# Optimization experiments

Hardware: AMD Instinct MI355X
Metric: run time of the kernel (lower is better)

## Reference

```python
import jax, jax.numpy as jnp
import numpy as np

EMBED_SIZE = 1024
HEADS = 16
HEAD_DIM = EMBED_SIZE // HEADS


def setup_inputs() -> dict:
    key = jax.random.key(0)
    k1, k2, k3, k4 = jax.random.split(key, 4)
    N, L = 4, 2048
    return {
        "values": jax.random.normal(k1, (N, L, EMBED_SIZE), dtype=jnp.float32),
        "keys": jax.random.normal(k2, (N, L, EMBED_SIZE), dtype=jnp.float32),
        "query": jax.random.normal(k3, (N, L, EMBED_SIZE), dtype=jnp.float32),
        "w_out": jax.random.normal(k4, (EMBED_SIZE, EMBED_SIZE), dtype=jnp.float32) * (1.0 / np.sqrt(EMBED_SIZE)),
        "b_out": jnp.zeros((EMBED_SIZE,), dtype=jnp.float32),
    }


def reference(values, keys, query, w_out, b_out):
    N, q_len, _ = query.shape
    v_len = values.shape[1]
    k_len = keys.shape[1]
    # split heads: (N, L, H, D). NOTE: source never applies the per-head
    # q/k/v Linear layers in forward, so raw inputs are used directly.
    v = values.reshape(N, v_len, HEADS, HEAD_DIM)
    k = keys.reshape(N, k_len, HEADS, HEAD_DIM)
    q = query.reshape(N, q_len, HEADS, HEAD_DIM)
    # energy: (N, H, Q, K); scale by sqrt(embed_size) as in the source
    energy = jnp.einsum('nqhd,nkhd->nhqk', q, k)
    attn = jax.nn.softmax(energy / jnp.sqrt(jnp.float32(EMBED_SIZE)), axis=3)
    out = jnp.einsum('nhql,nlhd->nqhd', attn, v).reshape(N, q_len, EMBED_SIZE)
    # fc_out: x @ W.T + b (torch Linear convention)
    return out @ w_out.T + b_out
```

## Files before the change

### kernel.cpp

```cpp
#include <hip/hip_runtime.h>
#include <hip/hip_bf16.h>

#define NB 4
#define LSEQ 2048
#define NH 16
#define HD 64
#define EMB 1024

typedef __attribute__((ext_vector_type(8))) short bf16x8;
typedef __attribute__((ext_vector_type(4))) float f32x4;
typedef __attribute__((ext_vector_type(16))) float f32x16;
typedef __attribute__((ext_vector_type(2))) unsigned int uint2v;

__device__ __forceinline__ unsigned short f2bf(float x) {
    union { float f; unsigned u; } v; v.f = x;
    unsigned r = v.u + 0x7fff + ((v.u >> 16) & 1);
    return (unsigned short)(r >> 16);
}

__device__ __forceinline__ float exp2_fast(float x) {
#if __has_builtin(__builtin_amdgcn_exp2f)
    return __builtin_amdgcn_exp2f(x);
#else
    float r; asm("v_exp_f32 %0, %1\n\ts_nop 1" : "=v"(r) : "v"(x)); return r;
#endif
}

__device__ __forceinline__ unsigned pack_bf2(float lo, float hi) {
    union { __hip_bfloat162 h2; unsigned u; } cv;
    cv.h2 = __float22bfloat162_rn(make_float2(lo, hi));
    return cv.u;
}

__device__ __forceinline__ void plswap(unsigned &a, unsigned &b) {
#if __has_builtin(__builtin_amdgcn_permlane32_swap)
    uint2v r = __builtin_amdgcn_permlane32_swap(a, b, false, false);
    a = r[0]; b = r[1];
#else
    asm volatile("s_nop 0\n\tv_permlane32_swap_b32 %0, %1\n\ts_nop 0"
                 : "+v"(a), "+v"(b));
#endif
}

__device__ __forceinline__ void async16(void* lds, const void* g) {
    __builtin_amdgcn_global_load_lds(
        (const __attribute__((address_space(1))) unsigned int*)g,
        (__attribute__((address_space(3))) unsigned int*)lds, 16, 0, 0);
}

__global__ void wconv_kernel(const float* __restrict__ Wf, unsigned short* __restrict__ Wb) {
    int i = (blockIdx.x * 256 + threadIdx.x) * 4;
    float4 v = *(const float4*)(Wf + i);
    ushort4 o = { f2bf(v.x), f2bf(v.y), f2bf(v.z), f2bf(v.w) };
    *(ushort4*)(Wb + i) = o;
}

__global__ void k_prep(const float* __restrict__ Kf, unsigned short* __restrict__ Kb) {
    int idx = blockIdx.x * 256 + threadIdx.x;
    int c   = idx & 7;
    int key = (idx >> 3) & 2047;
    int h   = (idx >> 14) & 15;
    int n   = idx >> 18;
    const float* src = Kf + (size_t)(n * LSEQ + key) * EMB + h * HD + c * 8;
    float4 a = *(const float4*)src;
    float4 b = *(const float4*)(src + 4);
    unsigned short* dst = Kb + (((size_t)(n * NH + h) * LSEQ + key) << 6)
                             + ((c ^ (key & 7)) << 3);
    ushort4 o0 = { f2bf(a.x), f2bf(a.y), f2bf(a.z), f2bf(a.w) };
    ushort4 o1 = { f2bf(b.x), f2bf(b.y), f2bf(b.z), f2bf(b.w) };
    *(ushort4*)dst = o0;
    *(ushort4*)(dst + 4) = o1;
}

__global__ void v_prep2(const float* __restrict__ Vf, unsigned short* __restrict__ Vt) {
    __shared__ float T[64][65];
    const int tid = threadIdx.x;
    const int b = blockIdx.x;
    const int kt = b & 31, h = (b >> 5) & 15, n = b >> 9;
    const float* src = Vf + (size_t)(n * LSEQ + kt * 64) * EMB + h * HD;
    unsigned short* dst = Vt + ((size_t)b << 12);

    for (int i = tid; i < 1024; i += 256) {
        const int key = i >> 4;
        const int c4  = (i & 15) * 4;
        const float4 v = *(const float4*)(src + (size_t)key * EMB + c4);
        T[key][c4 + 0] = v.x; T[key][c4 + 1] = v.y;
        T[key][c4 + 2] = v.z; T[key][c4 + 3] = v.w;
    }
    __syncthreads();
    for (int i = tid; i < 512; i += 256) {
        const int d = i >> 3, c = i & 7;
        ushort4 o0 = { f2bf(T[c * 8 + 0][d]), f2bf(T[c * 8 + 1][d]),
                       f2bf(T[c * 8 + 2][d]), f2bf(T[c * 8 + 3][d]) };
        ushort4 o1 = { f2bf(T[c * 8 + 4][d]), f2bf(T[c * 8 + 5][d]),
                       f2bf(T[c * 8 + 6][d]), f2bf(T[c * 8 + 7][d]) };
        unsigned short* p = dst + (d << 6) + ((c ^ (d & 7)) << 3);
        *(ushort4*)p = o0;
        *(ushort4*)(p + 4) = o1;
    }
}

__global__ __launch_bounds__(256, 2)
void attn11_kernel(const float* __restrict__ Qq, const unsigned short* __restrict__ Kb,
                   const unsigned short* __restrict__ Vt, unsigned short* __restrict__ X)
{
    __shared__ unsigned short Kl[2][4096];
    __shared__ unsigned short Vl[2][4096];

    const int tid  = threadIdx.x;
    const int lane = tid & 63;
    const int w    = tid >> 6;
    const int l31  = lane & 31;
    const int hl   = lane >> 5;
    const int swz7 = lane & 7;
    const int l    = ((blockIdx.x & 7) << 6) + (blockIdx.x >> 3);
    const int nh   = l >> 3;
    const int qtile = l & 7;
    const int n = nh >> 4, h = nh & 15;
    const int qrow0 = qtile * 256 + w * 64;

    bf16x8 ones;
    #pragma unroll
    for (int e = 0; e < 8; ++e) ones[e] = (short)0x3F80;

    const float qscale = 0.03125f * 1.44269504f;
    bf16x8 qf[2][4];
    #pragma unroll
    for (int g = 0; g < 2; ++g) {
        const float* qp = Qq + (size_t)(n * LSEQ + qrow0 + g * 32 + l31) * EMB + h * HD + hl * 8;
        #pragma unroll
        for (int dk = 0; dk < 4; ++dk) {
            bf16x8 t;
            #pragma unroll
            for (int e = 0; e < 8; ++e) t[e] = (short)f2bf(qp[dk * 16 + e] * qscale);
            qf[g][dk] = t;
        }
    }

    f32x16 oaccT[2][2];
    f32x16 lacc[2];
    #pragma unroll
    for (int g = 0; g < 2; ++g) {
        #pragma unroll
        for (int e = 0; e < 16; ++e) lacc[g][e] = 0.f;
        #pragma unroll
        for (int db = 0; db < 2; ++db)
            #pragma unroll
            for (int e = 0; e < 16; ++e) oaccT[g][db][e] = 0.f;
    }

    const unsigned short* kg0 = Kb + ((size_t)nh << 17);
    const unsigned short* vg0 = Vt + ((size_t)nh << 17);
    const int t8 = tid << 3;

    async16(&Kl[0][t8],        kg0 + t8);
    async16(&Kl[0][t8 + 2048], kg0 + t8 + 2048);
    async16(&Vl[0][t8],        vg0 + t8);
    async16(&Vl[0][t8 + 2048], vg0 + t8 + 2048);
    asm volatile("s_waitcnt vmcnt(0)" ::: "memory");
    __syncthreads();

    int cur = 0;
    for (int kt = 0; kt < LSEQ / 64; ++kt) {
        if (kt + 1 < LSEQ / 64) {
            const unsigned short* kg = kg0 + ((kt + 1) << 12) + t8;
            const unsigned short* vg = vg0 + ((kt + 1) << 12) + t8;
            async16(&Kl[cur ^ 1][t8],        kg);
            async16(&Kl[cur ^ 1][t8 + 2048], kg + 2048);
            async16(&Vl[cur ^ 1][t8],        vg);
            async16(&Vl[cur ^ 1][t8 + 2048], vg + 2048);
        }

        #pragma unroll
        for (int kb = 0; kb < 2; ++kb) {
            f32x16 sk[2];
            #pragma unroll
            for (int g = 0; g < 2; ++g)
                #pragma unroll
                for (int e = 0; e < 16; ++e) sk[g][e] = 0.f;
            #pragma unroll
            for (int dk = 0; dk < 4; ++dk) {
                bf16x8 ka = *(const bf16x8*)&Kl[cur][((kb * 32 + l31) << 6) + (((2 * dk + hl) ^ swz7) << 3)];
                #pragma unroll
                for (int g = 0; g < 2; ++g)
                    sk[g] = __builtin_amdgcn_mfma_f32_32x32x16_bf16(ka, qf[g][dk], sk[g], 0, 0, 0);
            }

            unsigned wgt[2][4][2];
            #pragma unroll
            for (int g = 0; g < 2; ++g) {
                float p[16];
                #pragma unroll
                for (int e = 0; e < 16; ++e) p[e] = exp2_fast(sk[g][e]);
                #pragma unroll
                for (int gg = 0; gg < 4; ++gg) {
                    wgt[g][gg][0] = pack_bf2(p[4 * gg + 0], p[4 * gg + 1]);
                    wgt[g][gg][1] = pack_bf2(p[4 * gg + 2], p[4 * gg + 3]);
                }
                plswap(wgt[g][0][0], wgt[g][1][0]); plswap(wgt[g][0][1], wgt[g][1][1]);
                plswap(wgt[g][2][0], wgt[g][3][0]); plswap(wgt[g][2][1], wgt[g][3][1]);
            }

            #pragma unroll
            for (int ks = 0; ks < 2; ++ks) {
                union { unsigned u[4]; bf16x8 v; } pu[2];
                #pragma unroll
                for (int g = 0; g < 2; ++g) {
                    pu[g].u[0] = wgt[g][2 * ks + 0][0];
                    pu[g].u[1] = wgt[g][2 * ks + 0][1];
                    pu[g].u[2] = wgt[g][2 * ks + 1][0];
                    pu[g].u[3] = wgt[g][2 * ks + 1][1];
                    lacc[g] = __builtin_amdgcn_mfma_f32_32x32x16_bf16(ones, pu[g].v, lacc[g], 0, 0, 0);
                }
                #pragma unroll
                for (int db = 0; db < 2; ++db) {
                    bf16x8 va = *(const bf16x8*)&Vl[cur][((db * 32 + l31) << 6) + (((4 * kb + 2 * ks + hl) ^ swz7) << 3)];
                    #pragma unroll
                    for (int g = 0; g < 2; ++g)
                        oaccT[g][db] = __builtin_amdgcn_mfma_f32_32x32x16_bf16(va, pu[g].v, oaccT[g][db], 0, 0, 0);
                }
            }
        }

        asm volatile("s_waitcnt vmcnt(0)" ::: "memory");
        __syncthreads();
        cur ^= 1;
    }

    #pragma unroll
    for (int g = 0; g < 2; ++g) {
        const float rcp = 1.0f / lacc[g][0];
        unsigned ow0[4][2], ow1[4][2];
        #pragma unroll
        for (int gg = 0; gg < 4; ++gg) {
            ow0[gg][0] = pack_bf2(oaccT[g][0][4 * gg + 0] * rcp, oaccT[g][0][4 * gg + 1] * rcp);
            ow0[gg][1] = pack_bf2(oaccT[g][0][4 * gg + 2] * rcp, oaccT[g][0][4 * gg + 3] * rcp);
            ow1[gg][0] = pack_bf2(oaccT[g][1][4 * gg + 0] * rcp, oaccT[g][1][4 * gg + 1] * rcp);
            ow1[gg][1] = pack_bf2(oaccT[g][1][4 * gg + 2] * rcp, oaccT[g][1][4 * gg + 3] * rcp);
        }
        #pragma unroll
        for (int gg = 0; gg < 4; ++gg) {
            plswap(ow0[gg][0], ow1[gg][0]);
            plswap(ow0[gg][1], ow1[gg][1]);
        }
        unsigned short* xrow = X + (size_t)(n * LSEQ + qrow0 + g * 32 + l31) * EMB + h * HD + hl * 32;
        #pragma unroll
        for (int gg = 0; gg < 4; ++gg) {
            uint4 st = { ow0[gg][0], ow0[gg][1], ow1[gg][0], ow1[gg][1] };
            *(uint4*)(xrow + 8 * gg) = st;
        }
    }
}

#define KPAD 72
#define PPAD 72

__global__ __launch_bounds__(256, 2)
void attn_kernel(const float* __restrict__ Vv, const float* __restrict__ Kk,
                 const float* __restrict__ Qq, unsigned short* __restrict__ X)
{
    __shared__ unsigned short Klds[64 * KPAD];
    __shared__ unsigned short Vtlds[64 * KPAD];
    __shared__ unsigned short Plds[4 * 16 * PPAD];

    const int tid  = threadIdx.x;
    const int lane = tid & 63;
    const int w    = tid >> 6;
    const int l15  = lane & 15;
    const int l4   = lane >> 4;
    const int qtile = blockIdx.x;
    const int nh    = blockIdx.y;
    const int n = nh >> 4, h = nh & 15;

    bf16x8 qf[2];
    {
        const int qrow = qtile * 64 + w * 16 + l15;
        const float* qp = Qq + (size_t)(n * LSEQ + qrow) * EMB + h * HD + l4 * 8;
        for (int kk = 0; kk < 2; ++kk) {
            bf16x8 t;
            #pragma unroll
            for (int e = 0; e < 8; ++e) t[e] = (short)f2bf(qp[kk * 32 + e] * 0.03125f);
            qf[kk] = t;
        }
    }

    f32x4 oacc[4];
    #pragma unroll
    for (int f = 0; f < 4; ++f) oacc[f] = (f32x4){0.f, 0.f, 0.f, 0.f};
    float mrun[4], lrun[4];
    #pragma unroll
    for (int r = 0; r < 4; ++r) { mrun[r] = -1e30f; lrun[r] = 0.f; }

    for (int kt = 0; kt < LSEQ / 64; ++kt) {
        __syncthreads();
        for (int i = tid; i < 1024; i += 256) {
            const int row = i >> 4;
            const int c4  = (i & 15) * 4;
            const size_t gb = (size_t)(n * LSEQ + kt * 64 + row) * EMB + h * HD + c4;
            const float4 kv = *(const float4*)(Kk + gb);
            const float4 vv = *(const float4*)(Vv + gb);
            ushort4 k4 = { f2bf(kv.x), f2bf(kv.y), f2bf(kv.z), f2bf(kv.w) };
            *(ushort4*)&Klds[row * KPAD + c4] = k4;
            Vtlds[(c4 + 0) * KPAD + row] = f2bf(vv.x);
            Vtlds[(c4 + 1) * KPAD + row] = f2bf(vv.y);
            Vtlds[(c4 + 2) * KPAD + row] = f2bf(vv.z);
            Vtlds[(c4 + 3) * KPAD + row] = f2bf(vv.w);
        }
        __syncthreads();

        f32x4 s[4];
        #pragma unroll
        for (int f = 0; f < 4; ++f) {
            f32x4 acc = (f32x4){0.f, 0.f, 0.f, 0.f};
            #pragma unroll
            for (int kk = 0; kk < 2; ++kk) {
                bf16x8 kb = *(const bf16x8*)&Klds[(f * 16 + l15) * KPAD + kk * 32 + l4 * 8];
                acc = __builtin_amdgcn_mfma_f32_16x16x32_bf16(qf[kk], kb, acc, 0, 0, 0);
            }
            s[f] = acc;
        }

        float mnew[4], corr[4];
        #pragma unroll
        for (int r = 0; r < 4; ++r) {
            float m0 = fmaxf(fmaxf(s[0][r], s[1][r]), fmaxf(s[2][r], s[3][r]));
            #pragma unroll
            for (int msk = 1; msk < 16; msk <<= 1) m0 = fmaxf(m0, __shfl_xor(m0, msk));
            mnew[r] = fmaxf(mrun[r], m0);
            corr[r] = __expf(mrun[r] - mnew[r]);
        }
        float psum[4] = {0.f, 0.f, 0.f, 0.f};
        #pragma unroll
        for (int f = 0; f < 4; ++f) {
            #pragma unroll
            for (int r = 0; r < 4; ++r) {
                float p = __expf(s[f][r] - mnew[r]);
                psum[r] += p;
                Plds[(w * 16 + l4 * 4 + r) * PPAD + f * 16 + l15] = f2bf(p);
            }
        }
        #pragma unroll
        for (int r = 0; r < 4; ++r) {
            float t = psum[r];
            #pragma unroll
            for (int msk = 1; msk < 16; msk <<= 1) t += __shfl_xor(t, msk);
            lrun[r] = lrun[r] * corr[r] + t;
            mrun[r] = mnew[r];
        }
        #pragma unroll
        for (int f = 0; f < 4; ++f) {
            #pragma unroll
            for (int r = 0; r < 4; ++r) oacc[f][r] *= corr[r];
        }
        __syncthreads();

        #pragma unroll
        for (int ks = 0; ks < 2; ++ks) {
            bf16x8 pa = *(const bf16x8*)&Plds[(w * 16 + l15) * PPAD + ks * 32 + l4 * 8];
            #pragma unroll
            for (int f = 0; f < 4; ++f) {
                bf16x8 vb = *(const bf16x8*)&Vtlds[(f * 16 + l15) * KPAD + ks * 32 + l4 * 8];
                oacc[f] = __builtin_amdgcn_mfma_f32_16x16x32_bf16(pa, vb, oacc[f], 0, 0, 0);
            }
        }
    }

    #pragma unroll
    for (int f = 0; f < 4; ++f) {
        #pragma unroll
        for (int r = 0; r < 4; ++r) {
            const int qrow = qtile * 64 + w * 16 + l4 * 4 + r;
            const float o = oacc[f][r] / lrun[r];
            X[(size_t)(n * LSEQ + qrow) * EMB + h * HD + f * 16 + l15] = f2bf(o);
        }
    }
}

__global__ __launch_bounds__(256, 2)
void proj4_kernel(const unsigned short* __restrict__ X, const unsigned short* __restrict__ Wb,
                  const float* __restrict__ bias, float* __restrict__ out)
{
    __shared__ unsigned short Al[2][8192];
    __shared__ unsigned short Bl[2][8192];

    const int tid  = threadIdx.x;
    const int lane = tid & 63;
    const int w    = tid >> 6;
    const int l15  = lane & 15;
    const int l4   = lane >> 4;
    const int bid  = blockIdx.x;
    const int bm   = (bid & 7) * 8 + ((bid >> 3) & 7);
    const int bn   = bid >> 6;
    const int wr = (w >> 1) * 64;
    const int wc = (w & 1) * 64;

    f32x4 acc[4][4];
    #pragma unroll
    for (int i = 0; i < 4; ++i)
        #pragma unroll
        for (int j = 0; j < 4; ++j) acc[i][j] = (f32x4){0.f, 0.f, 0.f, 0.f};

    int srow[4], soff[4];
    #pragma unroll
    for (int j = 0; j < 4; ++j) {
        const int cid = tid + j * 256;
        srow[j] = cid >> 3;
        const int c = cid & 7;
        soff[j] = ((c ^ (srow[j] & 7)) << 3);
    }

#define PROJ_STAGE(buf, k0)                                                          \
    {                                                                                \
        _Pragma("unroll")                                                            \
        for (int j = 0; j < 4; ++j) {                                                \
            const int cid = tid + j * 256;                                           \
            async16(&Al[buf][cid << 3],                                              \
                    &X [(size_t)(bm * 128 + srow[j]) * EMB + (k0) + soff[j]]);       \
            async16(&Bl[buf][cid << 3],                                              \
                    &Wb[(size_t)(bn * 128 + srow[j]) * EMB + (k0) + soff[j]]);       \
        }                                                                            \
    }

    PROJ_STAGE(0, 0)
    asm volatile("s_waitcnt vmcnt(0)" ::: "memory");
    __syncthreads();

    int cur = 0;
    for (int k0 = 0; k0 < EMB; k0 += 64) {
        if (k0 + 64 < EMB) PROJ_STAGE(cur ^ 1, k0 + 64)

        #pragma unroll
        for (int kk = 0; kk < 2; ++kk) {
            bf16x8 af[4], bfr[4];
            #pragma unroll
            for (int i = 0; i < 4; ++i) {
                const int row = wr + i * 16 + l15;
                af[i] = *(const bf16x8*)&Al[cur][(row << 6) + (((kk * 4 + l4) ^ (row & 7)) << 3)];
            }
            #pragma unroll
            for (int j = 0; j < 4; ++j) {
                const int row = wc + j * 16 + l15;
                bfr[j] = *(const bf16x8*)&Bl[cur][(row << 6) + (((kk * 4 + l4) ^ (row & 7)) << 3)];
            }
            #pragma unroll
            for (int i = 0; i < 4; ++i)
                #pragma unroll
                for (int j = 0; j < 4; ++j)
                    acc[i][j] = __builtin_amdgcn_mfma_f32_16x16x32_bf16(af[i], bfr[j], acc[i][j], 0, 0, 0);
        }

        asm volatile("s_waitcnt vmcnt(0)" ::: "memory");
        __syncthreads();
        cur ^= 1;
    }

    #pragma unroll
    for (int i = 0; i < 4; ++i) {
        const int row = bm * 128 + wr + i * 16 + l4 * 4;
        #pragma unroll
        for (int j = 0; j < 4; ++j) {
            const int col = bn * 128 + wc + j * 16 + l15;
            const float bj = bias[col];
            #pragma unroll
            for (int r = 0; r < 4; ++r)
                out[(size_t)(row + r) * EMB + col] = acc[i][j][r] + bj;
        }
    }
}

extern "C" void kernel_launch(void* const* d_in, const int* in_sizes, int n_in,
                              void* d_out, int out_size, void* d_ws, size_t ws_size,
                              hipStream_t stream) {
    const float* Vv   = (const float*)d_in[0];
    const float* Kk   = (const float*)d_in[1];
    const float* Qq   = (const float*)d_in[2];
    const float* Wf   = (const float*)d_in[3];
    const float* bias = (const float*)d_in[4];
    float* out = (float*)d_out;

    unsigned short* X  = (unsigned short*)d_ws;
    unsigned short* Wb = (unsigned short*)((char*)d_ws + (size_t)16 * 1024 * 1024);
    const size_t need = (size_t)50 * 1024 * 1024;

    wconv_kernel<<<dim3(EMB * EMB / 1024), 256, 0, stream>>>(Wf, Wb);

    if (ws_size >= need) {
        unsigned short* Kb = (unsigned short*)((char*)d_ws + (size_t)18 * 1024 * 1024);
        unsigned short* Vt = (unsigned short*)((char*)d_ws + (size_t)34 * 1024 * 1024);
        k_prep<<<dim3(4096), 256, 0, stream>>>(Kk, Kb);
        v_prep2<<<dim3(2048), 256, 0, stream>>>(Vv, Vt);
        attn11_kernel<<<dim3(512), 256, 0, stream>>>(Qq, Kb, Vt, X);
    } else {
        attn_kernel<<<dim3(LSEQ / 64, NB * NH), 256, 0, stream>>>(Vv, Kk, Qq, X);
    }

    proj4_kernel<<<dim3(512), 256, 0, stream>>>(X, Wb, bias, out);
}
```

Measured before the change: 131.5 us.

## Merge prep kernels into one launch and halve attention query tile per block

The weight, K and V conversion kernels become a single launch, with blocks dispatched to each job by block index. This removes two kernel launches and the gaps between them. The attention kernel now gives each wave 32 query rows instead of 64, doubling the grid to 1024 blocks and raising the launch bounds occupancy hint to 4. The goal is more parallelism and lower register pressure, at the cost of reusing each staged K/V tile across half as many queries, which doubles K/V traffic through LDS and global memory.

```diff
diff --git a/kernel.cpp b/kernel.cpp
--- a/kernel.cpp
+++ b/kernel.cpp
@@ -55,53 +55,67 @@
     *(ushort4*)(Wb + i) = o;
 }
 
-__global__ void k_prep(const float* __restrict__ Kf, unsigned short* __restrict__ Kb) {
-    int idx = blockIdx.x * 256 + threadIdx.x;
-    int c   = idx & 7;
-    int key = (idx >> 3) & 2047;
-    int h   = (idx >> 14) & 15;
-    int n   = idx >> 18;
-    const float* src = Kf + (size_t)(n * LSEQ + key) * EMB + h * HD + c * 8;
-    float4 a = *(const float4*)src;
-    float4 b = *(const float4*)(src + 4);
-    unsigned short* dst = Kb + (((size_t)(n * NH + h) * LSEQ + key) << 6)
-                             + ((c ^ (key & 7)) << 3);
-    ushort4 o0 = { f2bf(a.x), f2bf(a.y), f2bf(a.z), f2bf(a.w) };
-    ushort4 o1 = { f2bf(b.x), f2bf(b.y), f2bf(b.z), f2bf(b.w) };
-    *(ushort4*)dst = o0;
-    *(ushort4*)(dst + 4) = o1;
-}
-
-__global__ void v_prep2(const float* __restrict__ Vf, unsigned short* __restrict__ Vt) {
+__global__ void prep_all(const float* __restrict__ Wf, unsigned short* __restrict__ Wb,
+                         const float* __restrict__ Kf, unsigned short* __restrict__ Kb,
+                         const float* __restrict__ Vf, unsigned short* __restrict__ Vt)
+{
     __shared__ float T[64][65];
     const int tid = threadIdx.x;
     const int b = blockIdx.x;
-    const int kt = b & 31, h = (b >> 5) & 15, n = b >> 9;
-    const float* src = Vf + (size_t)(n * LSEQ + kt * 64) * EMB + h * HD;
-    unsigned short* dst = Vt + ((size_t)b << 12);
-
-    for (int i = tid; i < 1024; i += 256) {
-        const int key = i >> 4;
-        const int c4  = (i & 15) * 4;
-        const float4 v = *(const float4*)(src + (size_t)key * EMB + c4);
-        T[key][c4 + 0] = v.x; T[key][c4 + 1] = v.y;
-        T[key][c4 + 2] = v.z; T[key][c4 + 3] = v.w;
-    }
-    __syncthreads();
-    for (int i = tid; i < 512; i += 256) {
-        const int d = i >> 3, c = i & 7;
-        ushort4 o0 = { f2bf(T[c * 8 + 0][d]), f2bf(T[c * 8 + 1][d]),
-                       f2bf(T[c * 8 + 2][d]), f2bf(T[c * 8 + 3][d]) };
-        ushort4 o1 = { f2bf(T[c * 8 + 4][d]), f2bf(T[c * 8 + 5][d]),
-                       f2bf(T[c * 8 + 6][d]), f2bf(T[c * 8 + 7][d]) };
-        unsigned short* p = dst + (d << 6) + ((c ^ (d & 7)) << 3);
-        *(ushort4*)p = o0;
-        *(ushort4*)(p + 4) = o1;
-    }
-}
-
-__global__ __launch_bounds__(256, 2)
-void attn11_kernel(const float* __restrict__ Qq, const unsigned short* __restrict__ Kb,
+
+    if (b < 1024) {
+        int i = (b * 256 + tid) * 4;
+        float4 v = *(const float4*)(Wf + i);
+        ushort4 o = { f2bf(v.x), f2bf(v.y), f2bf(v.z), f2bf(v.w) };
+        *(ushort4*)(Wb + i) = o;
+        return;
+    }
+    if (b < 5120) {
+        int idx = (b - 1024) * 256 + tid;
+        int c   = idx & 7;
+        int key = (idx >> 3) & 2047;
+        int h   = (idx >> 14) & 15;
+        int n   = idx >> 18;
+        const float* src = Kf + (size_t)(n * LSEQ + key) * EMB + h * HD + c * 8;
+        float4 a = *(const float4*)src;
+        float4 bb = *(const float4*)(src + 4);
+        unsigned short* dst = Kb + (((size_t)(n * NH + h) * LSEQ + key) << 6)
+                                 + ((c ^ (key & 7)) << 3);
+        ushort4 o0 = { f2bf(a.x), f2bf(a.y), f2bf(a.z), f2bf(a.w) };
+        ushort4 o1 = { f2bf(bb.x), f2bf(bb.y), f2bf(bb.z), f2bf(bb.w) };
+        *(ushort4*)dst = o0;
+        *(ushort4*)(dst + 4) = o1;
+        return;
+    }
+    {
+        const int vb = b - 5120;
+        const int kt = vb & 31, h = (vb >> 5) & 15, n = vb >> 9;
+        const float* src = Vf + (size_t)(n * LSEQ + kt * 64) * EMB + h * HD;
+        unsigned short* dst = Vt + ((size_t)vb << 12);
+
+        for (int i = tid; i < 1024; i += 256) {
+            const int key = i >> 4;
+            const int c4  = (i & 15) * 4;
+            const float4 v = *(const float4*)(src + (size_t)key * EMB + c4);
+            T[key][c4 + 0] = v.x; T[key][c4 + 1] = v.y;
+            T[key][c4 + 2] = v.z; T[key][c4 + 3] = v.w;
+        }
+        __syncthreads();
+        for (int i = tid; i < 512; i += 256) {
+            const int d = i >> 3, c = i & 7;
+            ushort4 o0 = { f2bf(T[c * 8 + 0][d]), f2bf(T[c * 8 + 1][d]),
+                           f2bf(T[c * 8 + 2][d]), f2bf(T[c * 8 + 3][d]) };
+            ushort4 o1 = { f2bf(T[c * 8 + 4][d]), f2bf(T[c * 8 + 5][d]),
+                           f2bf(T[c * 8 + 6][d]), f2bf(T[c * 8 + 7][d]) };
+            unsigned short* p = dst + (d << 6) + ((c ^ (d & 7)) << 3);
+            *(ushort4*)p = o0;
+            *(ushort4*)(p + 4) = o1;
+        }
+    }
+}
+
+__global__ __launch_bounds__(256, 4)
+void attn12_kernel(const float* __restrict__ Qq, const unsigned short* __restrict__ Kb,
                    const unsigned short* __restrict__ Vt, unsigned short* __restrict__ X)
 {
     __shared__ unsigned short Kl[2][4096];
@@ -113,41 +127,37 @@
     const int l31  = lane & 31;
     const int hl   = lane >> 5;
     const int swz7 = lane & 7;
-    const int l    = ((blockIdx.x & 7) << 6) + (blockIdx.x >> 3);
-    const int nh   = l >> 3;
-    const int qtile = l & 7;
+    const int l    = ((blockIdx.x & 7) << 7) + (blockIdx.x >> 3);
+    const int nh   = l >> 4;
+    const int qtile = l & 15;
     const int n = nh >> 4, h = nh & 15;
-    const int qrow0 = qtile * 256 + w * 64;
+    const int qrow0 = qtile * 128 + w * 32;
 
     bf16x8 ones;
     #pragma unroll
     for (int e = 0; e < 8; ++e) ones[e] = (short)0x3F80;
 
     const float qscale = 0.03125f * 1.44269504f;
-    bf16x8 qf[2][4];
-    #pragma unroll
-    for (int g = 0; g < 2; ++g) {
-        const float* qp = Qq + (size_t)(n * LSEQ + qrow0 + g * 32 + l31) * EMB + h * HD + hl * 8;
+    bf16x8 qf[4];
+    {
+        const float* qp = Qq + (size_t)(n * LSEQ + qrow0 + l31) * EMB + h * HD + hl * 8;
         #pragma unroll
         for (int dk = 0; dk < 4; ++dk) {
             bf16x8 t;
             #pragma unroll
             for (int e = 0; e < 8; ++e) t[e] = (short)f2bf(qp[dk * 16 + e] * qscale);
-            qf[g][dk] = t;
-        }
-    }
-
-    f32x16 oaccT[2][2];
-    f32x16 lacc[2];
-    #pragma unroll
-    for (int g = 0; g < 2; ++g) {
-        #pragma unroll
-        for (int e = 0; e < 16; ++e) lacc[g][e] = 0.f;
-        #pragma unroll
-        for (int db = 0; db < 2; ++db)
-            #pragma unroll
-            for (int e = 0; e < 16; ++e) oaccT[g][db][e] = 0.f;
-    }
+            qf[dk] = t;
+        }
+    }
+
+    f32x16 oaccT[2];
+    f32x16 lacc;
+    #pragma unroll
+    for (int e = 0; e < 16; ++e) lacc[e] = 0.f;
+    #pragma unroll
+    for (int db = 0; db < 2; ++db)
+        #pragma unroll
+        for (int e = 0; e < 16; ++e) oaccT[db][e] = 0.f;
 
     const unsigned short* kg0 = Kb + ((size_t)nh << 17);
     const unsigned short* vg0 = Vt + ((size_t)nh << 17);
@@ -173,51 +183,39 @@
 
         #pragma unroll
         for (int kb = 0; kb < 2; ++kb) {
-            f32x16 sk[2];
-            #pragma unroll
-            for (int g = 0; g < 2; ++g)
-                #pragma unroll
-                for (int e = 0; e < 16; ++e) sk[g][e] = 0.f;
+            f32x16 sk;
+            #pragma unroll
+            for (int e = 0; e < 16; ++e) sk[e] = 0.f;
             #pragma unroll
             for (int dk = 0; dk < 4; ++dk) {
                 bf16x8 ka = *(const bf16x8*)&Kl[cur][((kb * 32 + l31) << 6) + (((2 * dk + hl) ^ swz7) << 3)];
-                #pragma unroll
-                for (int g = 0; g < 2; ++g)
-                    sk[g] = __builtin_amdgcn_mfma_f32_32x32x16_bf16(ka, qf[g][dk], sk[g], 0, 0, 0);
-            }
-
-            unsigned wgt[2][4][2];
-            #pragma unroll
-            for (int g = 0; g < 2; ++g) {
-                float p[16];
-                #pragma unroll
-                for (int e = 0; e < 16; ++e) p[e] = exp2_fast(sk[g][e]);
-                #pragma unroll
-                for (int gg = 0; gg < 4; ++gg) {
-                    wgt[g][gg][0] = pack_bf2(p[4 * gg + 0], p[4 * gg + 1]);
-                    wgt[g][gg][1] = pack_bf2(p[4 * gg + 2], p[4 * gg + 3]);
-                }
-                plswap(wgt[g][0][0], wgt[g][1][0]); plswap(wgt[g][0][1], wgt[g][1][1]);
-                plswap(wgt[g][2][0], wgt[g][3][0]); plswap(wgt[g][2][1], wgt[g][3][1]);
-            }
+                sk = __builtin_amdgcn_mfma_f32_32x32x16_bf16(ka, qf[dk], sk, 0, 0, 0);
+            }
+
+            float p[16];
+            #pragma unroll
+            for (int e = 0; e < 16; ++e) p[e] = exp2_fast(sk[e]);
+            unsigned wgt[4][2];
+            #pragma unroll
+            for (int gg = 0; gg < 4; ++gg) {
+                wgt[gg][0] = pack_bf2(p[4 * gg + 0], p[4 * gg + 1]);
+                wgt[gg][1] = pack_bf2(p[4 * gg + 2], p[4 * gg + 3]);
+            }
+            plswap(wgt[0][0], wgt[1][0]); plswap(wgt[0][1], wgt[1][1]);
+            plswap(wgt[2][0], wgt[3][0]); plswap(wgt[2][1], wgt[3][1]);
 
             #pragma unroll
             for (int ks = 0; ks < 2; ++ks) {
-                union { unsigned u[4]; bf16x8 v; } pu[2];
-                #pragma unroll
-                for (int g = 0; g < 2; ++g) {
-                    pu[g].u[0] = wgt[g][2 * ks + 0][0];
-                    pu[g].u[1] = wgt[g][2 * ks + 0][1];
-                    pu[g].u[2] = wgt[g][2 * ks + 1][0];
-                    pu[g].u[3] = wgt[g][2 * ks + 1][1];
-                    lacc[g] = __builtin_amdgcn_mfma_f32_32x32x16_bf16(ones, pu[g].v, lacc[g], 0, 0, 0);
-                }
+                union { unsigned u[4]; bf16x8 v; } pu;
+                pu.u[0] = wgt[2 * ks + 0][0];
+                pu.u[1] = wgt[2 * ks + 0][1];
+                pu.u[2] = wgt[2 * ks + 1][0];
+                pu.u[3] = wgt[2 * ks + 1][1];
+                lacc = __builtin_amdgcn_mfma_f32_32x32x16_bf16(ones, pu.v, lacc, 0, 0, 0);
                 #pragma unroll
                 for (int db = 0; db < 2; ++db) {
                     bf16x8 va = *(const bf16x8*)&Vl[cur][((db * 32 + l31) << 6) + (((4 * kb + 2 * ks + hl) ^ swz7) << 3)];
-                    #pragma unroll
-                    for (int g = 0; g < 2; ++g)
-                        oaccT[g][db] = __builtin_amdgcn_mfma_f32_32x32x16_bf16(va, pu[g].v, oaccT[g][db], 0, 0, 0);
+                    oaccT[db] = __builtin_amdgcn_mfma_f32_32x32x16_bf16(va, pu.v, oaccT[db], 0, 0, 0);
                 }
             }
         }
@@ -227,23 +225,22 @@
         cur ^= 1;
     }
 
-    #pragma unroll
-    for (int g = 0; g < 2; ++g) {
-        const float rcp = 1.0f / lacc[g][0];
+    {
+        const float rcp = 1.0f / lacc[0];
         unsigned ow0[4][2], ow1[4][2];
         #pragma unroll
         for (int gg = 0; gg < 4; ++gg) {
-            ow0[gg][0] = pack_bf2(oaccT[g][0][4 * gg + 0] * rcp, oaccT[g][0][4 * gg + 1] * rcp);
-            ow0[gg][1] = pack_bf2(oaccT[g][0][4 * gg + 2] * rcp, oaccT[g][0][4 * gg + 3] * rcp);
-            ow1[gg][0] = pack_bf2(oaccT[g][1][4 * gg + 0] * rcp, oaccT[g][1][4 * gg + 1] * rcp);
-            ow1[gg][1] = pack_bf2(oaccT[g][1][4 * gg + 2] * rcp, oaccT[g][1][4 * gg + 3] * rcp);
+            ow0[gg][0] = pack_bf2(oaccT[0][4 * gg + 0] * rcp, oaccT[0][4 * gg + 1] * rcp);
+            ow0[gg][1] = pack_bf2(oaccT[0][4 * gg + 2] * rcp, oaccT[0][4 * gg + 3] * rcp);
+            ow1[gg][0] = pack_bf2(oaccT[1][4 * gg + 0] * rcp, oaccT[1][4 * gg + 1] * rcp);
+            ow1[gg][1] = pack_bf2(oaccT[1][4 * gg + 2] * rcp, oaccT[1][4 * gg + 3] * rcp);
         }
         #pragma unroll
         for (int gg = 0; gg < 4; ++gg) {
             plswap(ow0[gg][0], ow1[gg][0]);
             plswap(ow0[gg][1], ow1[gg][1]);
         }
-        unsigned short* xrow = X + (size_t)(n * LSEQ + qrow0 + g * 32 + l31) * EMB + h * HD + hl * 32;
+        unsigned short* xrow = X + (size_t)(n * LSEQ + qrow0 + l31) * EMB + h * HD + hl * 32;
         #pragma unroll
         for (int gg = 0; gg < 4; ++gg) {
             uint4 st = { ow0[gg][0], ow0[gg][1], ow1[gg][0], ow1[gg][1] };
@@ -482,15 +479,13 @@
     unsigned short* Wb = (unsigned short*)((char*)d_ws + (size_t)16 * 1024 * 1024);
     const size_t need = (size_t)50 * 1024 * 1024;
 
-    wconv_kernel<<<dim3(EMB * EMB / 1024), 256, 0, stream>>>(Wf, Wb);
-
     if (ws_size >= need) {
         unsigned short* Kb = (unsigned short*)((char*)d_ws + (size_t)18 * 1024 * 1024);
         unsigned short* Vt = (unsigned short*)((char*)d_ws + (size_t)34 * 1024 * 1024);
-        k_prep<<<dim3(4096), 256, 0, stream>>>(Kk, Kb);
-        v_prep2<<<dim3(2048), 256, 0, stream>>>(Vv, Vt);
-        attn11_kernel<<<dim3(512), 256, 0, stream>>>(Qq, Kb, Vt, X);
+        prep_all<<<dim3(7168), 256, 0, stream>>>(Wf, Wb, Kk, Kb, Vv, Vt);
+        attn12_kernel<<<dim3(1024), 256, 0, stream>>>(Qq, Kb, Vt, X);
     } else {
+        wconv_kernel<<<dim3(EMB * EMB / 1024), 256, 0, stream>>>(Wf, Wb);
         attn_kernel<<<dim3(LSEQ / 64, NB * NH), 256, 0, stream>>>(Vv, Kk, Qq, X);
     }
 
```

New measurement: 136.1 us. +3.5%, slower.

## Merge prep kernels into one launch and triple-buffer K/V loads in attention

Applied to the files above, without the earlier changes.

Combines the weight conversion, K layout and V transpose kernels into a single launch that dispatches on block index, removing two kernel launches and their inter-kernel gaps. The attention kernel now keeps three LDS stages for K/V and prefetches two tiles ahead, waiting only for the oldest tile's loads instead of draining all outstanding loads each iteration. This raises LDS use per block from 32KB to 48KB, which may affect occupancy at two blocks per CU. It also swaps __syncthreads for a raw s_barrier.

```diff
diff --git a/kernel.cpp b/kernel.cpp
--- a/kernel.cpp
+++ b/kernel.cpp
@@ -55,57 +55,71 @@
     *(ushort4*)(Wb + i) = o;
 }
 
-__global__ void k_prep(const float* __restrict__ Kf, unsigned short* __restrict__ Kb) {
-    int idx = blockIdx.x * 256 + threadIdx.x;
-    int c   = idx & 7;
-    int key = (idx >> 3) & 2047;
-    int h   = (idx >> 14) & 15;
-    int n   = idx >> 18;
-    const float* src = Kf + (size_t)(n * LSEQ + key) * EMB + h * HD + c * 8;
-    float4 a = *(const float4*)src;
-    float4 b = *(const float4*)(src + 4);
-    unsigned short* dst = Kb + (((size_t)(n * NH + h) * LSEQ + key) << 6)
-                             + ((c ^ (key & 7)) << 3);
-    ushort4 o0 = { f2bf(a.x), f2bf(a.y), f2bf(a.z), f2bf(a.w) };
-    ushort4 o1 = { f2bf(b.x), f2bf(b.y), f2bf(b.z), f2bf(b.w) };
-    *(ushort4*)dst = o0;
-    *(ushort4*)(dst + 4) = o1;
-}
-
-__global__ void v_prep2(const float* __restrict__ Vf, unsigned short* __restrict__ Vt) {
+__global__ void prep_all(const float* __restrict__ Wf, unsigned short* __restrict__ Wb,
+                         const float* __restrict__ Kf, unsigned short* __restrict__ Kb,
+                         const float* __restrict__ Vf, unsigned short* __restrict__ Vt)
+{
     __shared__ float T[64][65];
     const int tid = threadIdx.x;
     const int b = blockIdx.x;
-    const int kt = b & 31, h = (b >> 5) & 15, n = b >> 9;
-    const float* src = Vf + (size_t)(n * LSEQ + kt * 64) * EMB + h * HD;
-    unsigned short* dst = Vt + ((size_t)b << 12);
-
-    for (int i = tid; i < 1024; i += 256) {
-        const int key = i >> 4;
-        const int c4  = (i & 15) * 4;
-        const float4 v = *(const float4*)(src + (size_t)key * EMB + c4);
-        T[key][c4 + 0] = v.x; T[key][c4 + 1] = v.y;
-        T[key][c4 + 2] = v.z; T[key][c4 + 3] = v.w;
-    }
-    __syncthreads();
-    for (int i = tid; i < 512; i += 256) {
-        const int d = i >> 3, c = i & 7;
-        ushort4 o0 = { f2bf(T[c * 8 + 0][d]), f2bf(T[c * 8 + 1][d]),
-                       f2bf(T[c * 8 + 2][d]), f2bf(T[c * 8 + 3][d]) };
-        ushort4 o1 = { f2bf(T[c * 8 + 4][d]), f2bf(T[c * 8 + 5][d]),
-                       f2bf(T[c * 8 + 6][d]), f2bf(T[c * 8 + 7][d]) };
-        unsigned short* p = dst + (d << 6) + ((c ^ (d & 7)) << 3);
-        *(ushort4*)p = o0;
-        *(ushort4*)(p + 4) = o1;
+
+    if (b < 1024) {
+        int i = (b * 256 + tid) * 4;
+        float4 v = *(const float4*)(Wf + i);
+        ushort4 o = { f2bf(v.x), f2bf(v.y), f2bf(v.z), f2bf(v.w) };
+        *(ushort4*)(Wb + i) = o;
+        return;
+    }
+    if (b < 5120) {
+        int idx = (b - 1024) * 256 + tid;
+        int c   = idx & 7;
+        int key = (idx >> 3) & 2047;
+        int h   = (idx >> 14) & 15;
+        int n   = idx >> 18;
+        const float* src = Kf + (size_t)(n * LSEQ + key) * EMB + h * HD + c * 8;
+        float4 a = *(const float4*)src;
+        float4 bb = *(const float4*)(src + 4);
+        unsigned short* dst = Kb + (((size_t)(n * NH + h) * LSEQ + key) << 6)
+                                 + ((c ^ (key & 7)) << 3);
+        ushort4 o0 = { f2bf(a.x), f2bf(a.y), f2bf(a.z), f2bf(a.w) };
+        ushort4 o1 = { f2bf(bb.x), f2bf(bb.y), f2bf(bb.z), f2bf(bb.w) };
+        *(ushort4*)dst = o0;
+        *(ushort4*)(dst + 4) = o1;
+        return;
+    }
+    {
+        const int vb = b - 5120;
+        const int kt = vb & 31, h = (vb >> 5) & 15, n = vb >> 9;
+        const float* src = Vf + (size_t)(n * LSEQ + kt * 64) * EMB + h * HD;
+        unsigned short* dst = Vt + ((size_t)vb << 12);
+
+        for (int i = tid; i < 1024; i += 256) {
+            const int key = i >> 4;
+            const int c4  = (i & 15) * 4;
+            const float4 v = *(const float4*)(src + (size_t)key * EMB + c4);
+            T[key][c4 + 0] = v.x; T[key][c4 + 1] = v.y;
+            T[key][c4 + 2] = v.z; T[key][c4 + 3] = v.w;
+        }
+        __syncthreads();
+        for (int i = tid; i < 512; i += 256) {
+            const int d = i >> 3, c = i & 7;
+            ushort4 o0 = { f2bf(T[c * 8 + 0][d]), f2bf(T[c * 8 + 1][d]),
+                           f2bf(T[c * 8 + 2][d]), f2bf(T[c * 8 + 3][d]) };
+            ushort4 o1 = { f2bf(T[c * 8 + 4][d]), f2bf(T[c * 8 + 5][d]),
+                           f2bf(T[c * 8 + 6][d]), f2bf(T[c * 8 + 7][d]) };
+            unsigned short* p = dst + (d << 6) + ((c ^ (d & 7)) << 3);
+            *(ushort4*)p = o0;
+            *(ushort4*)(p + 4) = o1;
+        }
     }
 }
 
 __global__ __launch_bounds__(256, 2)
-void attn11_kernel(const float* __restrict__ Qq, const unsigned short* __restrict__ Kb,
+void attn13_kernel(const float* __restrict__ Qq, const unsigned short* __restrict__ Kb,
                    const unsigned short* __restrict__ Vt, unsigned short* __restrict__ X)
 {
-    __shared__ unsigned short Kl[2][4096];
-    __shared__ unsigned short Vl[2][4096];
+    __shared__ unsigned short Kl[3][4096];
+    __shared__ unsigned short Vl[3][4096];
 
     const int tid  = threadIdx.x;
     const int lane = tid & 63;
@@ -153,22 +167,26 @@
     const unsigned short* vg0 = Vt + ((size_t)nh << 17);
     const int t8 = tid << 3;
 
-    async16(&Kl[0][t8],        kg0 + t8);
-    async16(&Kl[0][t8 + 2048], kg0 + t8 + 2048);
-    async16(&Vl[0][t8],        vg0 + t8);
-    async16(&Vl[0][t8 + 2048], vg0 + t8 + 2048);
-    asm volatile("s_waitcnt vmcnt(0)" ::: "memory");
-    __syncthreads();
+#define ATTN_STAGE(buf, kt)                                                  \
+    {                                                                        \
+        const unsigned short* kg = kg0 + ((kt) << 12) + t8;                  \
+        const unsigned short* vg = vg0 + ((kt) << 12) + t8;                  \
+        async16(&Kl[buf][t8],        kg);                                    \
+        async16(&Kl[buf][t8 + 2048], kg + 2048);                             \
+        async16(&Vl[buf][t8],        vg);                                    \
+        async16(&Vl[buf][t8 + 2048], vg + 2048);                             \
+    }
+
+    ATTN_STAGE(0, 0)
+    ATTN_STAGE(1, 1)
+    asm volatile("s_waitcnt vmcnt(4)" ::: "memory");
+    __builtin_amdgcn_s_barrier();
 
     int cur = 0;
     for (int kt = 0; kt < LSEQ / 64; ++kt) {
-        if (kt + 1 < LSEQ / 64) {
-            const unsigned short* kg = kg0 + ((kt + 1) << 12) + t8;
-            const unsigned short* vg = vg0 + ((kt + 1) << 12) + t8;
-            async16(&Kl[cur ^ 1][t8],        kg);
-            async16(&Kl[cur ^ 1][t8 + 2048], kg + 2048);
-            async16(&Vl[cur ^ 1][t8],        vg);
-            async16(&Vl[cur ^ 1][t8 + 2048], vg + 2048);
+        if (kt + 2 < LSEQ / 64) {
+            const int pre = cur >= 1 ? cur - 1 : cur + 2;
+            ATTN_STAGE(pre, kt + 2)
         }
 
         #pragma unroll
@@ -222,9 +240,13 @@
             }
         }
 
-        asm volatile("s_waitcnt vmcnt(0)" ::: "memory");
-        __syncthreads();
-        cur ^= 1;
+        if (kt + 2 < LSEQ / 64) {
+            asm volatile("s_waitcnt vmcnt(4)" ::: "memory");
+        } else {
+            asm volatile("s_waitcnt vmcnt(0)" ::: "memory");
+        }
+        __builtin_amdgcn_s_barrier();
+        cur = cur < 2 ? cur + 1 : 0;
     }
 
     #pragma unroll
@@ -482,15 +504,13 @@
     unsigned short* Wb = (unsigned short*)((char*)d_ws + (size_t)16 * 1024 * 1024);
     const size_t need = (size_t)50 * 1024 * 1024;
 
-    wconv_kernel<<<dim3(EMB * EMB / 1024), 256, 0, stream>>>(Wf, Wb);
-
     if (ws_size >= need) {
         unsigned short* Kb = (unsigned short*)((char*)d_ws + (size_t)18 * 1024 * 1024);
         unsigned short* Vt = (unsigned short*)((char*)d_ws + (size_t)34 * 1024 * 1024);
-        k_prep<<<dim3(4096), 256, 0, stream>>>(Kk, Kb);
-        v_prep2<<<dim3(2048), 256, 0, stream>>>(Vv, Vt);
-        attn11_kernel<<<dim3(512), 256, 0, stream>>>(Qq, Kb, Vt, X);
+        prep_all<<<dim3(7168), 256, 0, stream>>>(Wf, Wb, Kk, Kb, Vv, Vt);
+        attn13_kernel<<<dim3(512), 256, 0, stream>>>(Qq, Kb, Vt, X);
     } else {
+        wconv_kernel<<<dim3(EMB * EMB / 1024), 256, 0, stream>>>(Wf, Wb);
         attn_kernel<<<dim3(LSEQ / 64, NB * NH), 256, 0, stream>>>(Vv, Kk, Qq, X);
     }
 
```

Result: faster. 128.0 us (-2.7%).
